# Performance work log

Measured on AMD Instinct MI355X. Metric: run time of the kernel, lower is better.

The kernel has to match this reference:

```python
import jax, jax.numpy as jnp
import numpy as np

E, H, V = 512, 1024, 32000
T_IN, T_DEC, B = 128, 128, 64
SOS = 1
WIPE_IDS = jnp.array([2, 3, 4])  # <EOS>, '\u56fe', '\u6298'


def gru_cell(x, h, Wih, Whh, bih, bhh):
    # torch nn.GRU cell math
    gi = x @ Wih.T + bih  # [B, 3H]
    gh = h @ Whh.T + bhh  # [B, 3H]
    i_r, i_z, i_n = jnp.split(gi, 3, axis=-1)
    h_r, h_z, h_n = jnp.split(gh, 3, axis=-1)
    r = jax.nn.sigmoid(i_r + h_r)
    z = jax.nn.sigmoid(i_z + h_z)
    n = jnp.tanh(i_n + r * h_n)
    return (1.0 - z) * n + z * h


def setup_inputs() -> dict:
    key = jax.random.key(0)
    ks = jax.random.split(key, 20)
    f = lambda k, shape: jax.random.normal(k, shape, jnp.float32) * 0.05
    inp = {
        'emb': f(ks[0], (V, E)),
        'enc_Wih': f(ks[1], (3 * H, E)), 'enc_Whh': f(ks[2], (3 * H, H)),
        'enc_bih': f(ks[3], (3 * H,)), 'enc_bhh': f(ks[4], (3 * H,)),
        'attn_W': f(ks[5], (T_IN, E + H)), 'attn_b': f(ks[6], (T_IN,)),
        'comb_W': f(ks[7], (H, E + H)), 'comb_b': f(ks[8], (H,)),
        'dec_Wih': f(ks[9], (3 * H, H)), 'dec_Whh': f(ks[10], (3 * H, H)),
        'dec_bih': f(ks[11], (3 * H,)), 'dec_bhh': f(ks[12], (3 * H,)),
        'out_W': f(ks[13], (V, H)), 'out_b': f(ks[14], (V,)),
        'src_tokens': jax.random.randint(ks[15], (B, T_IN), 0, V, jnp.int32),
        'tgt_tokens': jax.random.randint(ks[16], (B, T_DEC), 0, V, jnp.int32),
    }
    # pack_padded_sequence needs lengths sorted descending with max == T_IN
    sl = jax.random.randint(ks[17], (B,), 1, T_IN + 1, jnp.int32).at[0].set(T_IN)
    inp['src_lengths'] = jnp.sort(sl)[::-1]
    tl = jax.random.randint(ks[18], (B,), 1, T_DEC + 1, jnp.int32).at[0].set(T_DEC)
    inp['tgt_lengths'] = tl
    return inp


def reference(emb, enc_Wih, enc_Whh, enc_bih, enc_bhh, attn_W, attn_b,
              comb_W, comb_b, dec_Wih, dec_Whh, dec_bih, dec_bhh,
              out_W, out_b, src_tokens, src_lengths, tgt_tokens, tgt_lengths):
    # ---------------- Encoder (packed GRU semantics) ----------------
    x = emb[src_tokens]  # [B, T_IN, E]  (dropout is eval-mode identity)
    valid = jnp.arange(T_IN)[None, :] < src_lengths[:, None]  # [B, T_IN]

    def enc_step(h, inp):
        xt, vt = inp  # [B,E], [B]
        hn = gru_cell(xt, h, enc_Wih, enc_Whh, enc_bih, enc_bhh)
        h = jnp.where(vt[:, None], hn, h)          # freeze hidden past length
        out = jnp.where(vt[:, None], hn, 0.0)      # pad_packed zeros past length
        return h, out

    h0 = jnp.zeros((B, H), emb.dtype)
    enc_h, enc_out = jax.lax.scan(enc_step, h0, (x.transpose(1, 0, 2), valid.T))
    enc_out = enc_out.transpose(1, 0, 2)  # [B, T_IN, H]
    enc_out = jax.nn.log_softmax(enc_out, axis=1)  # LogSoftmax(dim=1) over time, as in source

    # ---------------- Attention decoder with teacher forcing ----------------
    sos = jnp.full((B,), SOS, src_tokens.dtype)

    def dec_step(carry, inp):
        h, prev = carry
        di, tgt_t = inp
        e = emb[prev]  # [B, E]
        union = jnp.concatenate([e, h], axis=-1)  # [B, E+H]
        aw = jax.nn.softmax(union @ attn_W.T + attn_b, axis=-1)  # [B, T_IN]
        info = jnp.einsum('bt,bth->bh', aw, enc_out)  # bmm
        comb = jax.nn.relu(jnp.concatenate([e, info], axis=-1) @ comb_W.T + comb_b)
        h = gru_cell(comb, h, dec_Wih, dec_Whh, dec_bih, dec_bhh)
        logits = h @ out_W.T + out_b  # [B, V]
        m = di < tgt_lengths  # [B] wipeEOS condition: now_len < length[i]
        wiped = jnp.where(m[:, None], 0.0, logits[:, WIPE_IDS])
        logits = logits.at[:, WIPE_IDS].set(wiped)
        pred_t = jnp.argmax(logits, axis=-1)
        ce = -jax.nn.log_softmax(logits, axis=-1)[jnp.arange(B), tgt_t]
        mf = m.astype(logits.dtype)
        step_loss = jnp.sum(ce * mf) / jnp.sum(mf)  # masked_select(...).mean()
        return (h, tgt_t), (pred_t, step_loss)

    (_, _), (preds, losses) = jax.lax.scan(
        dec_step, (enc_h, sos), (jnp.arange(T_DEC), tgt_tokens.T))
    return preds.T, jnp.sum(losses)
```

## Files before the change

kernel.cpp:

```cpp
#include <hip/hip_runtime.h>
#include <math.h>

typedef long long i64;

#define B_    64
#define TIN   128
#define TDEC  128
#define E_    512
#define H_    1024
#define V_    32000
#define H3    3072
#define EH    1536
#define NROWS 8192
#define BH    (B_ * H_)

__device__ inline unsigned int ordf(float v) {
  unsigned int u = __float_as_uint(v);
  return (u & 0x80000000u) ? ~u : (u | 0x80000000u);
}

__device__ __forceinline__ void fma16(float acc[4][4], float4 s, float4 w) {
  acc[0][0] = fmaf(s.x, w.x, acc[0][0]); acc[0][1] = fmaf(s.x, w.y, acc[0][1]);
  acc[0][2] = fmaf(s.x, w.z, acc[0][2]); acc[0][3] = fmaf(s.x, w.w, acc[0][3]);
  acc[1][0] = fmaf(s.y, w.x, acc[1][0]); acc[1][1] = fmaf(s.y, w.y, acc[1][1]);
  acc[1][2] = fmaf(s.y, w.z, acc[1][2]); acc[1][3] = fmaf(s.y, w.w, acc[1][3]);
  acc[2][0] = fmaf(s.z, w.x, acc[2][0]); acc[2][1] = fmaf(s.z, w.y, acc[2][1]);
  acc[2][2] = fmaf(s.z, w.z, acc[2][2]); acc[2][3] = fmaf(s.z, w.w, acc[2][3]);
  acc[3][0] = fmaf(s.w, w.x, acc[3][0]); acc[3][1] = fmaf(s.w, w.y, acc[3][1]);
  acc[3][2] = fmaf(s.w, w.z, acc[3][2]); acc[3][3] = fmaf(s.w, w.w, acc[3][3]);
}

__global__ void diag_fill(float* __restrict__ out, int n, float val) {
  int i = blockIdx.x * blockDim.x + threadIdx.x;
  if (i < n) out[i] = val;
}

__global__ void init_ws(float* __restrict__ hbuf, unsigned long long* __restrict__ amaxkey,
                        float* __restrict__ sumexp) {
  int i = blockIdx.x * blockDim.x + threadIdx.x;
  if (i < 2 * B_ * H_) hbuf[i] = 0.f;
  if (i < NROWS) { amaxkey[i] = 0ull; sumexp[i] = 0.f; }
}

__global__ void prep_tokens(const int* __restrict__ src, const int* __restrict__ tgt,
                            int* __restrict__ tok_src, int* __restrict__ tok_prev) {
  int r = blockIdx.x * blockDim.x + threadIdx.x;
  if (r >= NROWS) return;
  int t = r >> 6, b = r & 63;
  tok_src[r]  = src[b * TIN + t];
  tok_prev[r] = (t == 0) ? 1 : tgt[b * TDEC + (t - 1)];
}

__global__ __launch_bounds__(256)
void gemm_gather(const float* __restrict__ emb, const int* __restrict__ tok,
                 const float* __restrict__ W, int wstride,
                 const float* __restrict__ bias,
                 float* __restrict__ C, int ldc) {
  __shared__ float As[32][132];
  __shared__ float Bs[32][136];
  __shared__ int toks[128];
  const int tid = threadIdx.x;
  const int tx = tid & 15, ty = tid >> 4;
  const int r0 = blockIdx.y * 128, n0 = blockIdx.x * 128;
  if (tid < 128) toks[tid] = tok[r0 + tid];
  __syncthreads();
  float acc[8][8];
#pragma unroll
  for (int i = 0; i < 8; ++i)
#pragma unroll
    for (int j = 0; j < 8; ++j) acc[i][j] = 0.f;

  for (int k0 = 0; k0 < E_; k0 += 32) {
#pragma unroll
    for (int j = 0; j < 4; ++j) {
      int s = tid + 256 * j;
      int m = s >> 3, k4 = (s & 7) << 2;
      float4 v = *reinterpret_cast<const float4*>(&emb[(i64)toks[m] * E_ + k0 + k4]);
      As[k4 + 0][m] = v.x; As[k4 + 1][m] = v.y; As[k4 + 2][m] = v.z; As[k4 + 3][m] = v.w;
      float4 u = *reinterpret_cast<const float4*>(&W[(i64)(n0 + m) * wstride + k0 + k4]);
      Bs[k4 + 0][m] = u.x; Bs[k4 + 1][m] = u.y; Bs[k4 + 2][m] = u.z; Bs[k4 + 3][m] = u.w;
    }
    __syncthreads();
#pragma unroll
    for (int k = 0; k < 32; ++k) {
      float a[8], b[8];
      *(float4*)&a[0] = *(float4*)&As[k][ty * 4];
      *(float4*)&a[4] = *(float4*)&As[k][64 + ty * 4];
      *(float4*)&b[0] = *(float4*)&Bs[k][tx * 4];
      *(float4*)&b[4] = *(float4*)&Bs[k][64 + tx * 4];
#pragma unroll
      for (int i = 0; i < 8; ++i)
#pragma unroll
        for (int j = 0; j < 8; ++j)
          acc[i][j] = fmaf(a[i], b[j], acc[i][j]);
    }
    __syncthreads();
  }
#pragma unroll
  for (int i = 0; i < 8; ++i) {
    int rl = (i < 4) ? (ty * 4 + i) : (64 + ty * 4 + i - 4);
    int r = r0 + rl;
#pragma unroll
    for (int j = 0; j < 8; ++j) {
      int cl = (j < 4) ? (tx * 4 + j) : (64 + tx * 4 + j - 4);
      int c = n0 + cl;
      C[(i64)r * ldc + c] = acc[i][j] + bias[c];
    }
  }
}

__global__ __launch_bounds__(512)
void enc_step2(const float* __restrict__ h_prev, float* __restrict__ h_next,
               const float* __restrict__ emb, const int* __restrict__ tokS,
               const float* __restrict__ Wih, const float* __restrict__ Whh,
               const float* __restrict__ bih, const float* __restrict__ bhh,
               const int* __restrict__ src_len, float* __restrict__ EncRaw, int t) {
  __shared__ float S[64][68];
  __shared__ float WL[64 * 32];
  __shared__ float red[8 * 1024];
  __shared__ int toks[64];
  const int tid = threadIdx.x;
  const int n0 = blockIdx.x * 4;
  const int bg = tid & 15, ac = (tid >> 4) & 3, ks = tid >> 6;
  const int b0 = bg * 4;
  if (tid < 64) toks[tid] = tokS[t * B_ + tid];
  float acc[4][4] = {{0}};
  for (int ch = 0; ch < 24; ++ch) {
    const bool isE = ch < 8;
    const int k0 = (isE ? ch : ch - 8) * 64;
    __syncthreads();
    {
      int b = tid & 63, kb = (tid >> 6) * 8;
      const float* src = isE ? &emb[(i64)toks[b] * E_ + k0 + kb]
                             : &h_prev[(i64)b * H_ + k0 + kb];
      float4 v0 = *(const float4*)src;
      float4 v1 = *(const float4*)(src + 4);
      S[kb + 0][b] = v0.x; S[kb + 1][b] = v0.y; S[kb + 2][b] = v0.z; S[kb + 3][b] = v0.w;
      S[kb + 4][b] = v1.x; S[kb + 5][b] = v1.y; S[kb + 6][b] = v1.z; S[kb + 7][b] = v1.w;
    }
    if (tid < 192) {
      int lin = tid * 4;
      int row12 = lin >> 6, k4 = lin & 63;
      int m = row12 >> 2, c = row12 & 3;
      const float* W = isE ? Wih : Whh;
      const int K = isE ? E_ : H_;
      float4 w = *(const float4*)&W[(i64)(m * H_ + n0 + c) * K + k0 + k4];
      int slot = ((m ^ ((k4 >> 2) & 7)) << 2) + c;
      WL[(k4 + 0) * 32 + slot] = w.x;
      WL[(k4 + 1) * 32 + slot] = w.y;
      WL[(k4 + 2) * 32 + slot] = w.z;
      WL[(k4 + 3) * 32 + slot] = w.w;
    }
    __syncthreads();
    const bool active = (ac < 2) || (ac == 2 && isE) || (ac == 3 && !isE);
    if (active) {
      const int m = (ac < 2) ? ac : 2;
#pragma unroll
      for (int kk = ks * 8; kk < ks * 8 + 8; ++kk) {
        float4 sv = *(float4*)&S[kk][b0];
        float4 wv = *(float4*)&WL[kk * 32 + ((m ^ ((kk >> 2) & 7)) << 2)];
        fma16(acc, sv, wv);
      }
    }
  }
  __syncthreads();
#pragma unroll
  for (int bi = 0; bi < 4; ++bi)
#pragma unroll
    for (int c = 0; c < 4; ++c)
      red[ks * 1024 + ac * 256 + c * 64 + b0 + bi] = acc[bi][c];
  __syncthreads();
  if (tid < 256) {
    int b = tid & 63, c = tid >> 6, col = n0 + c;
    float sr = 0, sz = 0, gin = 0, ghn = 0;
#pragma unroll
    for (int k2 = 0; k2 < 8; ++k2) {
      sr  += red[k2 * 1024 +   0 + c * 64 + b];
      sz  += red[k2 * 1024 + 256 + c * 64 + b];
      gin += red[k2 * 1024 + 512 + c * 64 + b];
      ghn += red[k2 * 1024 + 768 + c * 64 + b];
    }
    float r = 1.f / (1.f + expf(-(sr + bih[col] + bhh[col])));
    float z = 1.f / (1.f + expf(-(sz + bih[H_ + col] + bhh[H_ + col])));
    float nn = tanhf(gin + bih[2 * H_ + col] + r * (ghn + bhh[2 * H_ + col]));
    float hpv = h_prev[(i64)b * H_ + col];
    float hnew = (1.f - z) * nn + z * hpv;
    bool valid = t < src_len[b];
    h_next[(i64)b * H_ + col] = valid ? hnew : hpv;
    EncRaw[((i64)b * TIN + t) * H_ + col] = valid ? hnew : 0.f;
  }
}

__global__ void ls_time(float* __restrict__ Enc) {
  int idx = blockIdx.x * blockDim.x + threadIdx.x;
  int b = idx >> 10, c = idx & 1023;
  const i64 base = (i64)b * TIN * H_ + c;
  float M = -INFINITY;
  for (int t = 0; t < TIN; ++t) M = fmaxf(M, Enc[base + (i64)t * H_]);
  float S = 0.f;
  for (int t = 0; t < TIN; ++t) S += expf(Enc[base + (i64)t * H_] - M);
  float lg = M + logf(S);
  for (int t = 0; t < TIN; ++t) Enc[base + (i64)t * H_] -= lg;
}

__global__ __launch_bounds__(512)
void attn_info2(const float* __restrict__ h_prev, const float* __restrict__ Ae,
                const float* __restrict__ attn_W, const float* __restrict__ EncLS,
                float* __restrict__ info, int t) {
  __shared__ float hl[H_];
  __shared__ float sc[TIN];
  __shared__ float inf2[512];
  const int b = blockIdx.x & 63, quarter = blockIdx.x >> 6;
  const int tid = threadIdx.x;
  if (tid < 256) {
    float4 v = *(const float4*)&h_prev[(i64)b * H_ + tid * 4];
    *(float4*)&hl[tid * 4] = v;
  }
  __syncthreads();
  const int w = tid >> 6, lane = tid & 63;
#pragma unroll
  for (int si = 0; si < 16; ++si) {
    int s = w * 16 + si;
    float p = 0.f;
#pragma unroll
    for (int jj = 0; jj < 16; ++jj) {
      int j = jj * 64 + lane;
      p = fmaf(hl[j], attn_W[(i64)s * EH + E_ + j], p);
    }
#pragma unroll
    for (int off = 32; off > 0; off >>= 1) p += __shfl_down(p, off);
    if (lane == 0) sc[s] = p + Ae[((i64)t * B_ + b) * TIN + s];
  }
  __syncthreads();
  if (tid < 64) {
    float v0 = sc[tid], v1 = sc[tid + 64];
    float mx = fmaxf(v0, v1);
#pragma unroll
    for (int off = 32; off > 0; off >>= 1) mx = fmaxf(mx, __shfl_xor(mx, off));
    float e0 = expf(v0 - mx), e1 = expf(v1 - mx);
    float ss = e0 + e1;
#pragma unroll
    for (int off = 32; off > 0; off >>= 1) ss += __shfl_xor(ss, off);
    sc[tid] = e0 / ss; sc[tid + 64] = e1 / ss;
  }
  __syncthreads();
  {
    int c = quarter * 256 + (tid & 255);
    int th = tid >> 8;
    float acc = 0.f;
    for (int t2 = th * 64; t2 < th * 64 + 64; ++t2)
      acc = fmaf(sc[t2], EncLS[((i64)b * TIN + t2) * H_ + c], acc);
    inf2[tid] = acc;
    __syncthreads();
    if (th == 0) info[(i64)b * H_ + c] = acc + inf2[tid + 256];
  }
}

__global__ __launch_bounds__(512)
void comb2(const float* __restrict__ info, const float* __restrict__ emb,
           const int* __restrict__ tokP, const float* __restrict__ comb_W,
           const float* __restrict__ comb_b, float* __restrict__ comb, int t) {
  __shared__ float S[64][68];
  __shared__ float WB[64 * 20];
  __shared__ float red[8 * 256];
  __shared__ int toks[64];
  const int tid = threadIdx.x;
  const int n0 = blockIdx.x * 4;
  const int bg = tid & 15, cs = (tid >> 4) & 3, ks = tid >> 6;
  const int b0 = bg * 4;
  if (tid < 64) toks[tid] = tokP[t * B_ + tid];
  float acc[4] = {0, 0, 0, 0};
  for (int ch = 0; ch < 24; ++ch) {
    const bool isE = ch < 8;
    const int k0 = (isE ? ch : ch - 8) * 64;
    __syncthreads();
    {
      int b = tid & 63, kb = (tid >> 6) * 8;
      const float* src = isE ? &emb[(i64)toks[b] * E_ + k0 + kb]
                             : &info[(i64)b * H_ + k0 + kb];
      float4 v0 = *(const float4*)src;
      float4 v1 = *(const float4*)(src + 4);
      S[kb + 0][b] = v0.x; S[kb + 1][b] = v0.y; S[kb + 2][b] = v0.z; S[kb + 3][b] = v0.w;
      S[kb + 4][b] = v1.x; S[kb + 5][b] = v1.y; S[kb + 6][b] = v1.z; S[kb + 7][b] = v1.w;
    }
    if (tid < 64) {
      int k = tid;
      i64 koff = (i64)(isE ? 0 : E_) + k0 + k;
      float4 w;
      w.x = comb_W[(i64)(n0 + 0) * EH + koff];
      w.y = comb_W[(i64)(n0 + 1) * EH + koff];
      w.z = comb_W[(i64)(n0 + 2) * EH + koff];
      w.w = comb_W[(i64)(n0 + 3) * EH + koff];
      *(float4*)&WB[k * 20] = w;
    }
    __syncthreads();
#pragma unroll
    for (int kk = ks * 8; kk < ks * 8 + 8; ++kk) {
      float4 sv = *(float4*)&S[kk][b0];
      float wv = WB[kk * 20 + cs];
      acc[0] = fmaf(sv.x, wv, acc[0]);
      acc[1] = fmaf(sv.y, wv, acc[1]);
      acc[2] = fmaf(sv.z, wv, acc[2]);
      acc[3] = fmaf(sv.w, wv, acc[3]);
    }
  }
  __syncthreads();
#pragma unroll
  for (int bi = 0; bi < 4; ++bi)
    red[ks * 256 + cs * 64 + b0 + bi] = acc[bi];
  __syncthreads();
  if (tid < 256) {
    int b = tid & 63, c = tid >> 6;
    float s = comb_b[n0 + c];
#pragma unroll
    for (int k2 = 0; k2 < 8; ++k2) s += red[k2 * 256 + c * 64 + b];
    comb[(i64)b * H_ + n0 + c] = fmaxf(s, 0.f);
  }
}

__global__ __launch_bounds__(512)
void dec_gru2(const float* __restrict__ h_prev, const float* __restrict__ comb,
              const float* __restrict__ Wih, const float* __restrict__ Whh,
              const float* __restrict__ bih, const float* __restrict__ bhh,
              float* __restrict__ h_out) {
  __shared__ float S1[64][68];
  __shared__ float S2[64][68];
  __shared__ float WL[64 * 32];
  __shared__ float red[8 * 1024];
  const int tid = threadIdx.x;
  const int n0 = blockIdx.x * 4;
  const int bg = tid & 15, ac = (tid >> 4) & 3, ks = tid >> 6;
  const int b0 = bg * 4;
  float acc[4][4] = {{0}};
  for (int ch = 0; ch < 16; ++ch) {
    const int k0 = ch * 64;
    __syncthreads();
    {
      int b = tid & 63, kb = (tid >> 6) * 8;
      const float* s1 = &h_prev[(i64)b * H_ + k0 + kb];
      const float* s2 = &comb[(i64)b * H_ + k0 + kb];
      float4 v0 = *(const float4*)s1, v1 = *(const float4*)(s1 + 4);
      S1[kb + 0][b] = v0.x; S1[kb + 1][b] = v0.y; S1[kb + 2][b] = v0.z; S1[kb + 3][b] = v0.w;
      S1[kb + 4][b] = v1.x; S1[kb + 5][b] = v1.y; S1[kb + 6][b] = v1.z; S1[kb + 7][b] = v1.w;
      float4 u0 = *(const float4*)s2, u1 = *(const float4*)(s2 + 4);
      S2[kb + 0][b] = u0.x; S2[kb + 1][b] = u0.y; S2[kb + 2][b] = u0.z; S2[kb + 3][b] = u0.w;
      S2[kb + 4][b] = u1.x; S2[kb + 5][b] = u1.y; S2[kb + 6][b] = u1.z; S2[kb + 7][b] = u1.w;
    }
    if (tid < 384) {
      int lin = tid * 4;
      int row24 = lin >> 6, k4 = lin & 63;
      int m = row24 >> 2, c = row24 & 3;
      int g = m >> 1;
      const float* W = (m & 1) ? Wih : Whh;
      float4 w = *(const float4*)&W[(i64)(g * H_ + n0 + c) * H_ + k0 + k4];
      int slot = ((m ^ ((k4 >> 2) & 7)) << 2) + c;
      WL[(k4 + 0) * 32 + slot] = w.x;
      WL[(k4 + 1) * 32 + slot] = w.y;
      WL[(k4 + 2) * 32 + slot] = w.z;
      WL[(k4 + 3) * 32 + slot] = w.w;
    }
    __syncthreads();
    if (ac < 2) {
#pragma unroll
      for (int kk = ks * 8; kk < ks * 8 + 8; ++kk) {
        int key = (kk >> 2) & 7;
        float4 h4 = *(float4*)&S1[kk][b0];
        float4 c4 = *(float4*)&S2[kk][b0];
        float4 wh = *(float4*)&WL[kk * 32 + (((2 * ac) ^ key) << 2)];
        float4 wi = *(float4*)&WL[kk * 32 + (((2 * ac + 1) ^ key) << 2)];
        fma16(acc, h4, wh);
        fma16(acc, c4, wi);
      }
    } else if (ac == 2) {
#pragma unroll
      for (int kk = ks * 8; kk < ks * 8 + 8; ++kk) {
        int key = (kk >> 2) & 7;
        float4 c4 = *(float4*)&S2[kk][b0];
        float4 wi = *(float4*)&WL[kk * 32 + ((5 ^ key) << 2)];
        fma16(acc, c4, wi);
      }
    } else {
#pragma unroll
      for (int kk = ks * 8; kk < ks * 8 + 8; ++kk) {
        int key = (kk >> 2) & 7;
        float4 h4 = *(float4*)&S1[kk][b0];
        float4 wh = *(float4*)&WL[kk * 32 + ((4 ^ key) << 2)];
        fma16(acc, h4, wh);
      }
    }
  }
  __syncthreads();
#pragma unroll
  for (int bi = 0; bi < 4; ++bi)
#pragma unroll
    for (int c = 0; c < 4; ++c)
      red[ks * 1024 + ac * 256 + c * 64 + b0 + bi] = acc[bi][c];
  __syncthreads();
  if (tid < 256) {
    int b = tid & 63, c = tid >> 6, col = n0 + c;
    float sr = 0, sz = 0, gin = 0, ghn = 0;
#pragma unroll
    for (int k2 = 0; k2 < 8; ++k2) {
      sr  += red[k2 * 1024 +   0 + c * 64 + b];
      sz  += red[k2 * 1024 + 256 + c * 64 + b];
      gin += red[k2 * 1024 + 512 + c * 64 + b];
      ghn += red[k2 * 1024 + 768 + c * 64 + b];
    }
    float r = 1.f / (1.f + expf(-(sr + bih[col] + bhh[col])));
    float z = 1.f / (1.f + expf(-(sz + bih[H_ + col] + bhh[H_ + col])));
    float nn = tanhf(gin + bih[2 * H_ + col] + r * (ghn + bhh[2 * H_ + col]));
    float hpv = h_prev[(i64)b * H_ + col];
    h_out[(i64)b * H_ + col] = (1.f - z) * nn + z * hpv;
  }
}

__global__ __launch_bounds__(256)
void logits_fused(const float* __restrict__ A, const float* __restrict__ Wout,
                  const float* __restrict__ outb, const int* __restrict__ tlen,
                  unsigned long long* __restrict__ amaxkey, float* __restrict__ sumexp) {
  __shared__ union {
    struct { float As[32][132]; float Bs[32][136]; } g;
    struct { float redm[128][17]; int redi[128][17]; float reds[128][17]; } r;
  } sh;
  const int tid = threadIdx.x;
  const int tx = tid & 15, ty = tid >> 4;
  const int r0 = blockIdx.y * 128, n0 = blockIdx.x * 128;
  float acc[8][8];
#pragma unroll
  for (int i = 0; i < 8; ++i)
#pragma unroll
    for (int j = 0; j < 8; ++j) acc[i][j] = 0.f;

  for (int k0 = 0; k0 < H_; k0 += 32) {
#pragma unroll
    for (int j = 0; j < 4; ++j) {
      int s = tid + 256 * j;
      int m = s >> 3, k4 = (s & 7) << 2;
      float4 v = *reinterpret_cast<const float4*>(&A[(i64)(r0 + m) * H_ + k0 + k4]);
      sh.g.As[k4 + 0][m] = v.x; sh.g.As[k4 + 1][m] = v.y;
      sh.g.As[k4 + 2][m] = v.z; sh.g.As[k4 + 3][m] = v.w;
      float4 u = *reinterpret_cast<const float4*>(&Wout[(i64)(n0 + m) * H_ + k0 + k4]);
      sh.g.Bs[k4 + 0][m] = u.x; sh.g.Bs[k4 + 1][m] = u.y;
      sh.g.Bs[k4 + 2][m] = u.z; sh.g.Bs[k4 + 3][m] = u.w;
    }
    __syncthreads();
#pragma unroll
    for (int k = 0; k < 32; ++k) {
      float a[8], b[8];
      *(float4*)&a[0] = *(float4*)&sh.g.As[k][ty * 4];
      *(float4*)&a[4] = *(float4*)&sh.g.As[k][64 + ty * 4];
      *(float4*)&b[0] = *(float4*)&sh.g.Bs[k][tx * 4];
      *(float4*)&b[4] = *(float4*)&sh.g.Bs[k][64 + tx * 4];
#pragma unroll
      for (int i = 0; i < 8; ++i)
#pragma unroll
        for (int j = 0; j < 8; ++j)
          acc[i][j] = fmaf(a[i], b[j], acc[i][j]);
    }
    __syncthreads();
  }

  int cols[8], rloc[8];
#pragma unroll
  for (int j = 0; j < 8; ++j) cols[j] = n0 + ((j < 4) ? (tx * 4 + j) : (64 + tx * 4 + j - 4));
#pragma unroll
  for (int i = 0; i < 8; ++i) rloc[i] = (i < 4) ? (ty * 4 + i) : (64 + ty * 4 + i - 4);

#pragma unroll
  for (int i = 0; i < 8; ++i) {
    int r = r0 + rloc[i];
    int t = r >> 6, b = r & 63;
    bool m = t < tlen[b];
    float lm = -INFINITY; int li = 0x7fffffff; float ls = 0.f;
#pragma unroll
    for (int j = 0; j < 8; ++j) {
      float v = acc[i][j] + outb[cols[j]];
      if (m && cols[j] >= 2 && cols[j] <= 4) v = 0.f;
      ls += expf(v);
      if (v > lm || (v == lm && cols[j] < li)) { lm = v; li = cols[j]; }
    }
    sh.r.redm[rloc[i]][tx] = lm; sh.r.redi[rloc[i]][tx] = li; sh.r.reds[rloc[i]][tx] = ls;
  }
  __syncthreads();
  if (tid < 128) {
    float M = -INFINITY; int I = 0x7fffffff; float S = 0.f;
#pragma unroll
    for (int x = 0; x < 16; ++x) {
      float v = sh.r.redm[tid][x]; int id = sh.r.redi[tid][x];
      if (v > M || (v == M && id < I)) { M = v; I = id; }
      S += sh.r.reds[tid][x];
    }
    unsigned long long key = ((unsigned long long)ordf(M) << 32) | (0xFFFFFFFFu - (unsigned)I);
    atomicMax(&amaxkey[r0 + tid], key);
    atomicAdd(&sumexp[r0 + tid], S);
  }
}

__global__ void tlogit_kernel(const float* __restrict__ Hd, const float* __restrict__ Wout,
                              const float* __restrict__ outb, const int* __restrict__ tgt,
                              const int* __restrict__ tlen, float* __restrict__ tlog) {
  const int tid = threadIdx.x;
  const int w = tid >> 6, lane = tid & 63;
  const int r = blockIdx.x * 4 + w;
  const int t = r >> 6, b = r & 63;
  const int tg = tgt[b * TDEC + t];
  float p = 0.f;
#pragma unroll
  for (int jj = 0; jj < 16; ++jj) {
    int j = jj * 64 + lane;
    p = fmaf(Hd[(i64)r * H_ + j], Wout[(i64)tg * H_ + j], p);
  }
#pragma unroll
  for (int off = 32; off > 0; off >>= 1) p += __shfl_down(p, off);
  if (lane == 0) {
    float v = p + outb[tg];
    if ((t < tlen[b]) && tg >= 2 && tg <= 4) v = 0.f;
    tlog[r] = v;
  }
}

__global__ void merge_kernel(const unsigned long long* __restrict__ amaxkey,
                             const float* __restrict__ sumexp,
                             const float* __restrict__ tlog,
                             const int* __restrict__ tlen,
                             float* __restrict__ out, float* __restrict__ loss_t) {
  const int t = blockIdx.x, b = threadIdx.x;
  const int r = t * 64 + b;
  unsigned long long key = amaxkey[r];
  int I = (int)(0xFFFFFFFFu - (unsigned)(key & 0xFFFFFFFFull));
  float lse = logf(sumexp[r]);
  float ce = lse - tlog[r];
  bool m = t < tlen[b];
  out[b * TDEC + t] = (float)I;
  float num = m ? ce : 0.f;
  float den = m ? 1.f : 0.f;
#pragma unroll
  for (int off = 32; off > 0; off >>= 1) {
    num += __shfl_down(num, off);
    den += __shfl_down(den, off);
  }
  if (b == 0) loss_t[t] = num / den;
}

__global__ void loss_sum(const float* __restrict__ loss_t, float* __restrict__ out) {
  const int tid = threadIdx.x;
  float v = loss_t[tid];
#pragma unroll
  for (int off = 32; off > 0; off >>= 1) v += __shfl_down(v, off);
  __shared__ float ps[2];
  if ((tid & 63) == 0) ps[tid >> 6] = v;
  __syncthreads();
  if (tid == 0) out[B_ * TDEC] = ps[0] + ps[1];
}

extern "C" void kernel_launch(void* const* d_in, const int* in_sizes, int n_in,
                              void* d_out, int out_size, void* d_ws, size_t ws_size,
                              hipStream_t stream) {
  const float* emb     = (const float*)d_in[0];
  const float* enc_Wih = (const float*)d_in[1];
  const float* enc_Whh = (const float*)d_in[2];
  const float* enc_bih = (const float*)d_in[3];
  const float* enc_bhh = (const float*)d_in[4];
  const float* attn_W  = (const float*)d_in[5];
  const float* attn_b  = (const float*)d_in[6];
  const float* comb_W  = (const float*)d_in[7];
  const float* comb_b  = (const float*)d_in[8];
  const float* dec_Wih = (const float*)d_in[9];
  const float* dec_Whh = (const float*)d_in[10];
  const float* dec_bih = (const float*)d_in[11];
  const float* dec_bhh = (const float*)d_in[12];
  const float* out_W   = (const float*)d_in[13];
  const float* out_b   = (const float*)d_in[14];
  const int* src_tok = (const int*)d_in[15];
  const int* tgt_tok;
  const int* src_len;
  const int* tgt_len;
  if (in_sizes[16] == B_ * TDEC) {
    tgt_tok = (const int*)d_in[16];
    src_len = (const int*)d_in[17];
    tgt_len = (const int*)d_in[18];
  } else {
    src_len = (const int*)d_in[16];
    tgt_len = (const int*)d_in[17];
    tgt_tok = (const int*)d_in[18];
  }
  float* out = (float*)d_out;
  char* wsb = (char*)d_ws;
  size_t off = 0;
  auto alloc = [&](size_t bytes) { void* p = wsb + off; off += (bytes + 255) & ~(size_t)255; return p; };

  float* EncLS = (float*)alloc((size_t)NROWS * H_ * 4);
  float* hbuf  = (float*)alloc(2ull * B_ * H_ * 4);
  float* Ae    = (float*)alloc((size_t)NROWS * TIN * 4);
  float* Hdec  = (float*)alloc((size_t)NROWS * H_ * 4);
  float* info  = (float*)alloc((size_t)B_ * H_ * 4);
  float* comb  = (float*)alloc((size_t)B_ * H_ * 4);
  unsigned long long* amaxkey = (unsigned long long*)alloc((size_t)NROWS * 8);
  float* sumexp = (float*)alloc((size_t)NROWS * 4);
  float* tlog  = (float*)alloc((size_t)NROWS * 4);
  float* lossT = (float*)alloc(TDEC * 4);
  int* tokS    = (int*)alloc(NROWS * 4);
  int* tokP    = (int*)alloc(NROWS * 4);

  if (off > ws_size) {
    diag_fill<<<(out_size + 255) / 256, 256, 0, stream>>>(out, out_size, (float)ws_size);
    return;
  }

  init_ws<<<512, 256, 0, stream>>>(hbuf, amaxkey, sumexp);
  prep_tokens<<<32, 256, 0, stream>>>(src_tok, tgt_tok, tokS, tokP);
  gemm_gather<<<dim3(1, 64), 256, 0, stream>>>(emb, tokP, attn_W, EH, attn_b, Ae, TIN);

  for (int t = 0; t < TIN; ++t) {
    const float* hp = hbuf + (size_t)(t & 1) * BH;
    float* hn = hbuf + (size_t)((t + 1) & 1) * BH;
    enc_step2<<<256, 512, 0, stream>>>(hp, hn, emb, tokS, enc_Wih, enc_Whh,
                                       enc_bih, enc_bhh, src_len, EncLS, t);
  }
  ls_time<<<256, 256, 0, stream>>>(EncLS);

  for (int t = 0; t < TDEC; ++t) {
    const float* hp = (t == 0) ? hbuf : (Hdec + (i64)(t - 1) * BH);
    attn_info2<<<256, 512, 0, stream>>>(hp, Ae, attn_W, EncLS, info, t);
    comb2<<<256, 512, 0, stream>>>(info, emb, tokP, comb_W, comb_b, comb, t);
    dec_gru2<<<256, 512, 0, stream>>>(hp, comb, dec_Wih, dec_Whh, dec_bih, dec_bhh,
                                      Hdec + (i64)t * BH);
  }

  logits_fused<<<dim3(250, 64), 256, 0, stream>>>(Hdec, out_W, out_b, tgt_len, amaxkey, sumexp);
  tlogit_kernel<<<2048, 256, 0, stream>>>(Hdec, out_W, out_b, tgt_tok, tgt_len, tlog);
  merge_kernel<<<128, 64, 0, stream>>>(amaxkey, sumexp, tlog, tgt_len, out, lossT);
  loss_sum<<<1, 128, 0, stream>>>(lossT, out);
}
```

Measured before the change: 36.11 ms.

## Replace per-timestep kernel launches with persistent kernels using grid barriers

The encoder loop (128 launches) and the decoder loop (384 launches) each become one persistent kernel of 256 blocks. The kernel steps through time internally and synchronises all blocks with an atomic-counter grid barrier. The aim is to remove per-launch overhead and the kernel-boundary drains between dependent stages. The barrier relies on all 256 blocks being co-resident, otherwise it can deadlock, and each barrier spins on a global atomic.

```diff
diff --git a/kernel.cpp b/kernel.cpp
--- a/kernel.cpp
+++ b/kernel.cpp
@@ -30,16 +30,30 @@
   acc[3][2] = fmaf(s.w, w.z, acc[3][2]); acc[3][3] = fmaf(s.w, w.w, acc[3][3]);
 }
 
+__device__ __forceinline__ void grid_bar(int* bar, int target_mult) {
+  __syncthreads();
+  if (threadIdx.x == 0) {
+    __threadfence();
+    __hip_atomic_fetch_add(bar, 1, __ATOMIC_RELEASE, __HIP_MEMORY_SCOPE_AGENT);
+    const int target = target_mult * (int)gridDim.x;
+    while (__hip_atomic_load(bar, __ATOMIC_ACQUIRE, __HIP_MEMORY_SCOPE_AGENT) < target)
+      __builtin_amdgcn_s_sleep(1);
+    __threadfence();
+  }
+  __syncthreads();
+}
+
 __global__ void diag_fill(float* __restrict__ out, int n, float val) {
   int i = blockIdx.x * blockDim.x + threadIdx.x;
   if (i < n) out[i] = val;
 }
 
 __global__ void init_ws(float* __restrict__ hbuf, unsigned long long* __restrict__ amaxkey,
-                        float* __restrict__ sumexp) {
+                        float* __restrict__ sumexp, int* __restrict__ bars) {
   int i = blockIdx.x * blockDim.x + threadIdx.x;
   if (i < 2 * B_ * H_) hbuf[i] = 0.f;
   if (i < NROWS) { amaxkey[i] = 0ull; sumexp[i] = 0.f; }
+  if (i < 2) bars[i] = 0;
 }
 
 __global__ void prep_tokens(const int* __restrict__ src, const int* __restrict__ tgt,
@@ -110,84 +124,97 @@
 }
 
 __global__ __launch_bounds__(512)
-void enc_step2(const float* __restrict__ h_prev, float* __restrict__ h_next,
-               const float* __restrict__ emb, const int* __restrict__ tokS,
-               const float* __restrict__ Wih, const float* __restrict__ Whh,
-               const float* __restrict__ bih, const float* __restrict__ bhh,
-               const int* __restrict__ src_len, float* __restrict__ EncRaw, int t) {
-  __shared__ float S[64][68];
-  __shared__ float WL[64 * 32];
-  __shared__ float red[8 * 1024];
-  __shared__ int toks[64];
+void enc_persist(float* __restrict__ hbufs, const float* __restrict__ emb,
+                 const int* __restrict__ tokS,
+                 const float* __restrict__ Wih, const float* __restrict__ Whh,
+                 const float* __restrict__ bih, const float* __restrict__ bhh,
+                 const int* __restrict__ src_len, float* __restrict__ EncRaw,
+                 int* __restrict__ bar) {
+  __shared__ union {
+    struct {
+      float S[64][68];
+      float WL[64 * 32];
+      float red[8 * 1024];
+      int toks[64];
+    } e;
+  } sh;
   const int tid = threadIdx.x;
   const int n0 = blockIdx.x * 4;
   const int bg = tid & 15, ac = (tid >> 4) & 3, ks = tid >> 6;
   const int b0 = bg * 4;
-  if (tid < 64) toks[tid] = tokS[t * B_ + tid];
-  float acc[4][4] = {{0}};
-  for (int ch = 0; ch < 24; ++ch) {
-    const bool isE = ch < 8;
-    const int k0 = (isE ? ch : ch - 8) * 64;
+
+  for (int t = 0; t < TIN; ++t) {
+    const float* h_prev = hbufs + (size_t)(t & 1) * BH;
+    float* h_next = hbufs + (size_t)((t + 1) & 1) * BH;
+    if (tid < 64) sh.e.toks[tid] = tokS[t * B_ + tid];
+    float acc[4][4] = {{0}};
+    for (int ch = 0; ch < 24; ++ch) {
+      const bool isE = ch < 8;
+      const int k0 = (isE ? ch : ch - 8) * 64;
+      __syncthreads();
+      {
+        int b = tid & 63, kb = (tid >> 6) * 8;
+        const float* src = isE ? &emb[(i64)sh.e.toks[b] * E_ + k0 + kb]
+                               : &h_prev[(i64)b * H_ + k0 + kb];
+        float4 v0 = *(const float4*)src;
+        float4 v1 = *(const float4*)(src + 4);
+        sh.e.S[kb + 0][b] = v0.x; sh.e.S[kb + 1][b] = v0.y;
+        sh.e.S[kb + 2][b] = v0.z; sh.e.S[kb + 3][b] = v0.w;
+        sh.e.S[kb + 4][b] = v1.x; sh.e.S[kb + 5][b] = v1.y;
+        sh.e.S[kb + 6][b] = v1.z; sh.e.S[kb + 7][b] = v1.w;
+      }
+      if (tid < 192) {
+        int lin = tid * 4;
+        int row12 = lin >> 6, k4 = lin & 63;
+        int m = row12 >> 2, c = row12 & 3;
+        const float* W = isE ? Wih : Whh;
+        const int K = isE ? E_ : H_;
+        float4 w = *(const float4*)&W[(i64)(m * H_ + n0 + c) * K + k0 + k4];
+        int slot = ((m ^ ((k4 >> 2) & 7)) << 2) + c;
+        sh.e.WL[(k4 + 0) * 32 + slot] = w.x;
+        sh.e.WL[(k4 + 1) * 32 + slot] = w.y;
+        sh.e.WL[(k4 + 2) * 32 + slot] = w.z;
+        sh.e.WL[(k4 + 3) * 32 + slot] = w.w;
+      }
+      __syncthreads();
+      const bool active = (ac < 2) || (ac == 2 && isE) || (ac == 3 && !isE);
+      if (active) {
+        const int m = (ac < 2) ? ac : 2;
+#pragma unroll
+        for (int kk = ks * 8; kk < ks * 8 + 8; ++kk) {
+          float4 sv = *(float4*)&sh.e.S[kk][b0];
+          float4 wv = *(float4*)&sh.e.WL[kk * 32 + ((m ^ ((kk >> 2) & 7)) << 2)];
+          fma16(acc, sv, wv);
+        }
+      }
+    }
     __syncthreads();
-    {
-      int b = tid & 63, kb = (tid >> 6) * 8;
-      const float* src = isE ? &emb[(i64)toks[b] * E_ + k0 + kb]
-                             : &h_prev[(i64)b * H_ + k0 + kb];
-      float4 v0 = *(const float4*)src;
-      float4 v1 = *(const float4*)(src + 4);
-      S[kb + 0][b] = v0.x; S[kb + 1][b] = v0.y; S[kb + 2][b] = v0.z; S[kb + 3][b] = v0.w;
-      S[kb + 4][b] = v1.x; S[kb + 5][b] = v1.y; S[kb + 6][b] = v1.z; S[kb + 7][b] = v1.w;
-    }
-    if (tid < 192) {
-      int lin = tid * 4;
-      int row12 = lin >> 6, k4 = lin & 63;
-      int m = row12 >> 2, c = row12 & 3;
-      const float* W = isE ? Wih : Whh;
-      const int K = isE ? E_ : H_;
-      float4 w = *(const float4*)&W[(i64)(m * H_ + n0 + c) * K + k0 + k4];
-      int slot = ((m ^ ((k4 >> 2) & 7)) << 2) + c;
-      WL[(k4 + 0) * 32 + slot] = w.x;
-      WL[(k4 + 1) * 32 + slot] = w.y;
-      WL[(k4 + 2) * 32 + slot] = w.z;
-      WL[(k4 + 3) * 32 + slot] = w.w;
-    }
+#pragma unroll
+    for (int bi = 0; bi < 4; ++bi)
+#pragma unroll
+      for (int c = 0; c < 4; ++c)
+        sh.e.red[ks * 1024 + ac * 256 + c * 64 + b0 + bi] = acc[bi][c];
     __syncthreads();
-    const bool active = (ac < 2) || (ac == 2 && isE) || (ac == 3 && !isE);
-    if (active) {
-      const int m = (ac < 2) ? ac : 2;
-#pragma unroll
-      for (int kk = ks * 8; kk < ks * 8 + 8; ++kk) {
-        float4 sv = *(float4*)&S[kk][b0];
-        float4 wv = *(float4*)&WL[kk * 32 + ((m ^ ((kk >> 2) & 7)) << 2)];
-        fma16(acc, sv, wv);
-      }
-    }
-  }
-  __syncthreads();
-#pragma unroll
-  for (int bi = 0; bi < 4; ++bi)
-#pragma unroll
-    for (int c = 0; c < 4; ++c)
-      red[ks * 1024 + ac * 256 + c * 64 + b0 + bi] = acc[bi][c];
-  __syncthreads();
-  if (tid < 256) {
-    int b = tid & 63, c = tid >> 6, col = n0 + c;
-    float sr = 0, sz = 0, gin = 0, ghn = 0;
-#pragma unroll
-    for (int k2 = 0; k2 < 8; ++k2) {
-      sr  += red[k2 * 1024 +   0 + c * 64 + b];
-      sz  += red[k2 * 1024 + 256 + c * 64 + b];
-      gin += red[k2 * 1024 + 512 + c * 64 + b];
-      ghn += red[k2 * 1024 + 768 + c * 64 + b];
-    }
-    float r = 1.f / (1.f + expf(-(sr + bih[col] + bhh[col])));
-    float z = 1.f / (1.f + expf(-(sz + bih[H_ + col] + bhh[H_ + col])));
-    float nn = tanhf(gin + bih[2 * H_ + col] + r * (ghn + bhh[2 * H_ + col]));
-    float hpv = h_prev[(i64)b * H_ + col];
-    float hnew = (1.f - z) * nn + z * hpv;
-    bool valid = t < src_len[b];
-    h_next[(i64)b * H_ + col] = valid ? hnew : hpv;
-    EncRaw[((i64)b * TIN + t) * H_ + col] = valid ? hnew : 0.f;
+    if (tid < 256) {
+      int b = tid & 63, c = tid >> 6, col = n0 + c;
+      float sr = 0, sz = 0, gin = 0, ghn = 0;
+#pragma unroll
+      for (int k2 = 0; k2 < 8; ++k2) {
+        sr  += sh.e.red[k2 * 1024 +   0 + c * 64 + b];
+        sz  += sh.e.red[k2 * 1024 + 256 + c * 64 + b];
+        gin += sh.e.red[k2 * 1024 + 512 + c * 64 + b];
+        ghn += sh.e.red[k2 * 1024 + 768 + c * 64 + b];
+      }
+      float r = 1.f / (1.f + expf(-(sr + bih[col] + bhh[col])));
+      float z = 1.f / (1.f + expf(-(sz + bih[H_ + col] + bhh[H_ + col])));
+      float nn = tanhf(gin + bih[2 * H_ + col] + r * (ghn + bhh[2 * H_ + col]));
+      float hpv = h_prev[(i64)b * H_ + col];
+      float hnew = (1.f - z) * nn + z * hpv;
+      bool valid = t < src_len[b];
+      h_next[(i64)b * H_ + col] = valid ? hnew : hpv;
+      EncRaw[((i64)b * TIN + t) * H_ + col] = valid ? hnew : 0.f;
+    }
+    grid_bar(bar, t + 1);
   }
 }
 
@@ -204,213 +231,221 @@
 }
 
 __global__ __launch_bounds__(512)
-void attn_info2(const float* __restrict__ h_prev, const float* __restrict__ Ae,
-                const float* __restrict__ attn_W, const float* __restrict__ EncLS,
-                float* __restrict__ info, int t) {
-  __shared__ float hl[H_];
-  __shared__ float sc[TIN];
-  __shared__ float inf2[512];
-  const int b = blockIdx.x & 63, quarter = blockIdx.x >> 6;
+void dec_persist(const float* __restrict__ h0, float* __restrict__ Hdec,
+                 const float* __restrict__ emb, const int* __restrict__ tokP,
+                 const float* __restrict__ Ae, const float* __restrict__ attn_W,
+                 const float* __restrict__ EncLS,
+                 const float* __restrict__ comb_W, const float* __restrict__ comb_b,
+                 const float* __restrict__ Wih, const float* __restrict__ Whh,
+                 const float* __restrict__ bih, const float* __restrict__ bhh,
+                 float* __restrict__ info, float* __restrict__ comb,
+                 int* __restrict__ bar) {
+  __shared__ union {
+    struct { float hl[H_]; float sc[TIN]; float inf2[512]; } a;
+    struct { float S[64][68]; float WB[64 * 20]; float red[8 * 256]; int toks[64]; } b;
+    struct { float S1[64][68]; float S2[64][68]; float WL[64 * 32]; float red[8 * 1024]; } c;
+  } sh;
   const int tid = threadIdx.x;
-  if (tid < 256) {
-    float4 v = *(const float4*)&h_prev[(i64)b * H_ + tid * 4];
-    *(float4*)&hl[tid * 4] = v;
-  }
-  __syncthreads();
-  const int w = tid >> 6, lane = tid & 63;
-#pragma unroll
-  for (int si = 0; si < 16; ++si) {
-    int s = w * 16 + si;
-    float p = 0.f;
-#pragma unroll
-    for (int jj = 0; jj < 16; ++jj) {
-      int j = jj * 64 + lane;
-      p = fmaf(hl[j], attn_W[(i64)s * EH + E_ + j], p);
-    }
-#pragma unroll
-    for (int off = 32; off > 0; off >>= 1) p += __shfl_down(p, off);
-    if (lane == 0) sc[s] = p + Ae[((i64)t * B_ + b) * TIN + s];
-  }
-  __syncthreads();
-  if (tid < 64) {
-    float v0 = sc[tid], v1 = sc[tid + 64];
-    float mx = fmaxf(v0, v1);
-#pragma unroll
-    for (int off = 32; off > 0; off >>= 1) mx = fmaxf(mx, __shfl_xor(mx, off));
-    float e0 = expf(v0 - mx), e1 = expf(v1 - mx);
-    float ss = e0 + e1;
-#pragma unroll
-    for (int off = 32; off > 0; off >>= 1) ss += __shfl_xor(ss, off);
-    sc[tid] = e0 / ss; sc[tid + 64] = e1 / ss;
-  }
-  __syncthreads();
-  {
-    int c = quarter * 256 + (tid & 255);
-    int th = tid >> 8;
-    float acc = 0.f;
-    for (int t2 = th * 64; t2 < th * 64 + 64; ++t2)
-      acc = fmaf(sc[t2], EncLS[((i64)b * TIN + t2) * H_ + c], acc);
-    inf2[tid] = acc;
-    __syncthreads();
-    if (th == 0) info[(i64)b * H_ + c] = acc + inf2[tid + 256];
-  }
-}
-
-__global__ __launch_bounds__(512)
-void comb2(const float* __restrict__ info, const float* __restrict__ emb,
-           const int* __restrict__ tokP, const float* __restrict__ comb_W,
-           const float* __restrict__ comb_b, float* __restrict__ comb, int t) {
-  __shared__ float S[64][68];
-  __shared__ float WB[64 * 20];
-  __shared__ float red[8 * 256];
-  __shared__ int toks[64];
-  const int tid = threadIdx.x;
-  const int n0 = blockIdx.x * 4;
-  const int bg = tid & 15, cs = (tid >> 4) & 3, ks = tid >> 6;
-  const int b0 = bg * 4;
-  if (tid < 64) toks[tid] = tokP[t * B_ + tid];
-  float acc[4] = {0, 0, 0, 0};
-  for (int ch = 0; ch < 24; ++ch) {
-    const bool isE = ch < 8;
-    const int k0 = (isE ? ch : ch - 8) * 64;
-    __syncthreads();
+  int sync_i = 0;
+
+  for (int t = 0; t < TDEC; ++t) {
+    const float* h_prev = (t == 0) ? h0 : (Hdec + (i64)(t - 1) * BH);
+
     {
-      int b = tid & 63, kb = (tid >> 6) * 8;
-      const float* src = isE ? &emb[(i64)toks[b] * E_ + k0 + kb]
-                             : &info[(i64)b * H_ + k0 + kb];
-      float4 v0 = *(const float4*)src;
-      float4 v1 = *(const float4*)(src + 4);
-      S[kb + 0][b] = v0.x; S[kb + 1][b] = v0.y; S[kb + 2][b] = v0.z; S[kb + 3][b] = v0.w;
-      S[kb + 4][b] = v1.x; S[kb + 5][b] = v1.y; S[kb + 6][b] = v1.z; S[kb + 7][b] = v1.w;
-    }
-    if (tid < 64) {
-      int k = tid;
-      i64 koff = (i64)(isE ? 0 : E_) + k0 + k;
-      float4 w;
-      w.x = comb_W[(i64)(n0 + 0) * EH + koff];
-      w.y = comb_W[(i64)(n0 + 1) * EH + koff];
-      w.z = comb_W[(i64)(n0 + 2) * EH + koff];
-      w.w = comb_W[(i64)(n0 + 3) * EH + koff];
-      *(float4*)&WB[k * 20] = w;
-    }
-    __syncthreads();
-#pragma unroll
-    for (int kk = ks * 8; kk < ks * 8 + 8; ++kk) {
-      float4 sv = *(float4*)&S[kk][b0];
-      float wv = WB[kk * 20 + cs];
-      acc[0] = fmaf(sv.x, wv, acc[0]);
-      acc[1] = fmaf(sv.y, wv, acc[1]);
-      acc[2] = fmaf(sv.z, wv, acc[2]);
-      acc[3] = fmaf(sv.w, wv, acc[3]);
-    }
-  }
-  __syncthreads();
-#pragma unroll
-  for (int bi = 0; bi < 4; ++bi)
-    red[ks * 256 + cs * 64 + b0 + bi] = acc[bi];
-  __syncthreads();
-  if (tid < 256) {
-    int b = tid & 63, c = tid >> 6;
-    float s = comb_b[n0 + c];
-#pragma unroll
-    for (int k2 = 0; k2 < 8; ++k2) s += red[k2 * 256 + c * 64 + b];
-    comb[(i64)b * H_ + n0 + c] = fmaxf(s, 0.f);
-  }
-}
-
-__global__ __launch_bounds__(512)
-void dec_gru2(const float* __restrict__ h_prev, const float* __restrict__ comb,
-              const float* __restrict__ Wih, const float* __restrict__ Whh,
-              const float* __restrict__ bih, const float* __restrict__ bhh,
-              float* __restrict__ h_out) {
-  __shared__ float S1[64][68];
-  __shared__ float S2[64][68];
-  __shared__ float WL[64 * 32];
-  __shared__ float red[8 * 1024];
-  const int tid = threadIdx.x;
-  const int n0 = blockIdx.x * 4;
-  const int bg = tid & 15, ac = (tid >> 4) & 3, ks = tid >> 6;
-  const int b0 = bg * 4;
-  float acc[4][4] = {{0}};
-  for (int ch = 0; ch < 16; ++ch) {
-    const int k0 = ch * 64;
-    __syncthreads();
+      const int b = blockIdx.x & 63, quarter = blockIdx.x >> 6;
+      if (tid < 256) {
+        float4 v = *(const float4*)&h_prev[(i64)b * H_ + tid * 4];
+        *(float4*)&sh.a.hl[tid * 4] = v;
+      }
+      __syncthreads();
+      const int w = tid >> 6, lane = tid & 63;
+#pragma unroll
+      for (int si = 0; si < 16; ++si) {
+        int s = w * 16 + si;
+        float p = 0.f;
+#pragma unroll
+        for (int jj = 0; jj < 16; ++jj) {
+          int j = jj * 64 + lane;
+          p = fmaf(sh.a.hl[j], attn_W[(i64)s * EH + E_ + j], p);
+        }
+#pragma unroll
+        for (int off = 32; off > 0; off >>= 1) p += __shfl_down(p, off);
+        if (lane == 0) sh.a.sc[s] = p + Ae[((i64)t * B_ + b) * TIN + s];
+      }
+      __syncthreads();
+      if (tid < 64) {
+        float v0 = sh.a.sc[tid], v1 = sh.a.sc[tid + 64];
+        float mx = fmaxf(v0, v1);
+#pragma unroll
+        for (int off = 32; off > 0; off >>= 1) mx = fmaxf(mx, __shfl_xor(mx, off));
+        float e0 = expf(v0 - mx), e1 = expf(v1 - mx);
+        float ss = e0 + e1;
+#pragma unroll
+        for (int off = 32; off > 0; off >>= 1) ss += __shfl_xor(ss, off);
+        sh.a.sc[tid] = e0 / ss; sh.a.sc[tid + 64] = e1 / ss;
+      }
+      __syncthreads();
+      {
+        int c = quarter * 256 + (tid & 255);
+        int th = tid >> 8;
+        float acc = 0.f;
+        for (int t2 = th * 64; t2 < th * 64 + 64; ++t2)
+          acc = fmaf(sh.a.sc[t2], EncLS[((i64)b * TIN + t2) * H_ + c], acc);
+        sh.a.inf2[tid] = acc;
+        __syncthreads();
+        if (th == 0) info[(i64)b * H_ + c] = acc + sh.a.inf2[tid + 256];
+      }
+    }
+    grid_bar(bar, ++sync_i);
+
     {
-      int b = tid & 63, kb = (tid >> 6) * 8;
-      const float* s1 = &h_prev[(i64)b * H_ + k0 + kb];
-      const float* s2 = &comb[(i64)b * H_ + k0 + kb];
-      float4 v0 = *(const float4*)s1, v1 = *(const float4*)(s1 + 4);
-      S1[kb + 0][b] = v0.x; S1[kb + 1][b] = v0.y; S1[kb + 2][b] = v0.z; S1[kb + 3][b] = v0.w;
-      S1[kb + 4][b] = v1.x; S1[kb + 5][b] = v1.y; S1[kb + 6][b] = v1.z; S1[kb + 7][b] = v1.w;
-      float4 u0 = *(const float4*)s2, u1 = *(const float4*)(s2 + 4);
-      S2[kb + 0][b] = u0.x; S2[kb + 1][b] = u0.y; S2[kb + 2][b] = u0.z; S2[kb + 3][b] = u0.w;
-      S2[kb + 4][b] = u1.x; S2[kb + 5][b] = u1.y; S2[kb + 6][b] = u1.z; S2[kb + 7][b] = u1.w;
-    }
-    if (tid < 384) {
-      int lin = tid * 4;
-      int row24 = lin >> 6, k4 = lin & 63;
-      int m = row24 >> 2, c = row24 & 3;
-      int g = m >> 1;
-      const float* W = (m & 1) ? Wih : Whh;
-      float4 w = *(const float4*)&W[(i64)(g * H_ + n0 + c) * H_ + k0 + k4];
-      int slot = ((m ^ ((k4 >> 2) & 7)) << 2) + c;
-      WL[(k4 + 0) * 32 + slot] = w.x;
-      WL[(k4 + 1) * 32 + slot] = w.y;
-      WL[(k4 + 2) * 32 + slot] = w.z;
-      WL[(k4 + 3) * 32 + slot] = w.w;
-    }
-    __syncthreads();
-    if (ac < 2) {
-#pragma unroll
-      for (int kk = ks * 8; kk < ks * 8 + 8; ++kk) {
-        int key = (kk >> 2) & 7;
-        float4 h4 = *(float4*)&S1[kk][b0];
-        float4 c4 = *(float4*)&S2[kk][b0];
-        float4 wh = *(float4*)&WL[kk * 32 + (((2 * ac) ^ key) << 2)];
-        float4 wi = *(float4*)&WL[kk * 32 + (((2 * ac + 1) ^ key) << 2)];
-        fma16(acc, h4, wh);
-        fma16(acc, c4, wi);
-      }
-    } else if (ac == 2) {
-#pragma unroll
-      for (int kk = ks * 8; kk < ks * 8 + 8; ++kk) {
-        int key = (kk >> 2) & 7;
-        float4 c4 = *(float4*)&S2[kk][b0];
-        float4 wi = *(float4*)&WL[kk * 32 + ((5 ^ key) << 2)];
-        fma16(acc, c4, wi);
-      }
-    } else {
-#pragma unroll
-      for (int kk = ks * 8; kk < ks * 8 + 8; ++kk) {
-        int key = (kk >> 2) & 7;
-        float4 h4 = *(float4*)&S1[kk][b0];
-        float4 wh = *(float4*)&WL[kk * 32 + ((4 ^ key) << 2)];
-        fma16(acc, h4, wh);
-      }
-    }
-  }
-  __syncthreads();
-#pragma unroll
-  for (int bi = 0; bi < 4; ++bi)
-#pragma unroll
-    for (int c = 0; c < 4; ++c)
-      red[ks * 1024 + ac * 256 + c * 64 + b0 + bi] = acc[bi][c];
-  __syncthreads();
-  if (tid < 256) {
-    int b = tid & 63, c = tid >> 6, col = n0 + c;
-    float sr = 0, sz = 0, gin = 0, ghn = 0;
-#pragma unroll
-    for (int k2 = 0; k2 < 8; ++k2) {
-      sr  += red[k2 * 1024 +   0 + c * 64 + b];
-      sz  += red[k2 * 1024 + 256 + c * 64 + b];
-      gin += red[k2 * 1024 + 512 + c * 64 + b];
-      ghn += red[k2 * 1024 + 768 + c * 64 + b];
-    }
-    float r = 1.f / (1.f + expf(-(sr + bih[col] + bhh[col])));
-    float z = 1.f / (1.f + expf(-(sz + bih[H_ + col] + bhh[H_ + col])));
-    float nn = tanhf(gin + bih[2 * H_ + col] + r * (ghn + bhh[2 * H_ + col]));
-    float hpv = h_prev[(i64)b * H_ + col];
-    h_out[(i64)b * H_ + col] = (1.f - z) * nn + z * hpv;
+      const int n0 = blockIdx.x * 4;
+      const int bg = tid & 15, cs = (tid >> 4) & 3, ks = tid >> 6;
+      const int b0 = bg * 4;
+      if (tid < 64) sh.b.toks[tid] = tokP[t * B_ + tid];
+      float acc[4] = {0, 0, 0, 0};
+      for (int ch = 0; ch < 24; ++ch) {
+        const bool isE = ch < 8;
+        const int k0 = (isE ? ch : ch - 8) * 64;
+        __syncthreads();
+        {
+          int b = tid & 63, kb = (tid >> 6) * 8;
+          const float* src = isE ? &emb[(i64)sh.b.toks[b] * E_ + k0 + kb]
+                                 : &info[(i64)b * H_ + k0 + kb];
+          float4 v0 = *(const float4*)src;
+          float4 v1 = *(const float4*)(src + 4);
+          sh.b.S[kb + 0][b] = v0.x; sh.b.S[kb + 1][b] = v0.y;
+          sh.b.S[kb + 2][b] = v0.z; sh.b.S[kb + 3][b] = v0.w;
+          sh.b.S[kb + 4][b] = v1.x; sh.b.S[kb + 5][b] = v1.y;
+          sh.b.S[kb + 6][b] = v1.z; sh.b.S[kb + 7][b] = v1.w;
+        }
+        if (tid < 64) {
+          int k = tid;
+          i64 koff = (i64)(isE ? 0 : E_) + k0 + k;
+          float4 w;
+          w.x = comb_W[(i64)(n0 + 0) * EH + koff];
+          w.y = comb_W[(i64)(n0 + 1) * EH + koff];
+          w.z = comb_W[(i64)(n0 + 2) * EH + koff];
+          w.w = comb_W[(i64)(n0 + 3) * EH + koff];
+          *(float4*)&sh.b.WB[k * 20] = w;
+        }
+        __syncthreads();
+#pragma unroll
+        for (int kk = ks * 8; kk < ks * 8 + 8; ++kk) {
+          float4 sv = *(float4*)&sh.b.S[kk][b0];
+          float wv = sh.b.WB[kk * 20 + cs];
+          acc[0] = fmaf(sv.x, wv, acc[0]);
+          acc[1] = fmaf(sv.y, wv, acc[1]);
+          acc[2] = fmaf(sv.z, wv, acc[2]);
+          acc[3] = fmaf(sv.w, wv, acc[3]);
+        }
+      }
+      __syncthreads();
+#pragma unroll
+      for (int bi = 0; bi < 4; ++bi)
+        sh.b.red[ks * 256 + cs * 64 + b0 + bi] = acc[bi];
+      __syncthreads();
+      if (tid < 256) {
+        int b = tid & 63, c = tid >> 6;
+        float s = comb_b[n0 + c];
+#pragma unroll
+        for (int k2 = 0; k2 < 8; ++k2) s += sh.b.red[k2 * 256 + c * 64 + b];
+        comb[(i64)b * H_ + n0 + c] = fmaxf(s, 0.f);
+      }
+    }
+    grid_bar(bar, ++sync_i);
+
+    {
+      const int n0 = blockIdx.x * 4;
+      const int bg = tid & 15, ac = (tid >> 4) & 3, ks = tid >> 6;
+      const int b0 = bg * 4;
+      float acc[4][4] = {{0}};
+      for (int ch = 0; ch < 16; ++ch) {
+        const int k0 = ch * 64;
+        __syncthreads();
+        {
+          int b = tid & 63, kb = (tid >> 6) * 8;
+          const float* s1 = &h_prev[(i64)b * H_ + k0 + kb];
+          const float* s2 = &comb[(i64)b * H_ + k0 + kb];
+          float4 v0 = *(const float4*)s1, v1 = *(const float4*)(s1 + 4);
+          sh.c.S1[kb + 0][b] = v0.x; sh.c.S1[kb + 1][b] = v0.y;
+          sh.c.S1[kb + 2][b] = v0.z; sh.c.S1[kb + 3][b] = v0.w;
+          sh.c.S1[kb + 4][b] = v1.x; sh.c.S1[kb + 5][b] = v1.y;
+          sh.c.S1[kb + 6][b] = v1.z; sh.c.S1[kb + 7][b] = v1.w;
+          float4 u0 = *(const float4*)s2, u1 = *(const float4*)(s2 + 4);
+          sh.c.S2[kb + 0][b] = u0.x; sh.c.S2[kb + 1][b] = u0.y;
+          sh.c.S2[kb + 2][b] = u0.z; sh.c.S2[kb + 3][b] = u0.w;
+          sh.c.S2[kb + 4][b] = u1.x; sh.c.S2[kb + 5][b] = u1.y;
+          sh.c.S2[kb + 6][b] = u1.z; sh.c.S2[kb + 7][b] = u1.w;
+        }
+        if (tid < 384) {
+          int lin = tid * 4;
+          int row24 = lin >> 6, k4 = lin & 63;
+          int m = row24 >> 2, c = row24 & 3;
+          int g = m >> 1;
+          const float* W = (m & 1) ? Wih : Whh;
+          float4 w = *(const float4*)&W[(i64)(g * H_ + n0 + c) * H_ + k0 + k4];
+          int slot = ((m ^ ((k4 >> 2) & 7)) << 2) + c;
+          sh.c.WL[(k4 + 0) * 32 + slot] = w.x;
+          sh.c.WL[(k4 + 1) * 32 + slot] = w.y;
+          sh.c.WL[(k4 + 2) * 32 + slot] = w.z;
+          sh.c.WL[(k4 + 3) * 32 + slot] = w.w;
+        }
+        __syncthreads();
+        if (ac < 2) {
+#pragma unroll
+          for (int kk = ks * 8; kk < ks * 8 + 8; ++kk) {
+            int key = (kk >> 2) & 7;
+            float4 h4 = *(float4*)&sh.c.S1[kk][b0];
+            float4 c4 = *(float4*)&sh.c.S2[kk][b0];
+            float4 wh = *(float4*)&sh.c.WL[kk * 32 + (((2 * ac) ^ key) << 2)];
+            float4 wi = *(float4*)&sh.c.WL[kk * 32 + (((2 * ac + 1) ^ key) << 2)];
+            fma16(acc, h4, wh);
+            fma16(acc, c4, wi);
+          }
+        } else if (ac == 2) {
+#pragma unroll
+          for (int kk = ks * 8; kk < ks * 8 + 8; ++kk) {
+            int key = (kk >> 2) & 7;
+            float4 c4 = *(float4*)&sh.c.S2[kk][b0];
+            float4 wi = *(float4*)&sh.c.WL[kk * 32 + ((5 ^ key) << 2)];
+            fma16(acc, c4, wi);
+          }
+        } else {
+#pragma unroll
+          for (int kk = ks * 8; kk < ks * 8 + 8; ++kk) {
+            int key = (kk >> 2) & 7;
+            float4 h4 = *(float4*)&sh.c.S1[kk][b0];
+            float4 wh = *(float4*)&sh.c.WL[kk * 32 + ((4 ^ key) << 2)];
+            fma16(acc, h4, wh);
+          }
+        }
+      }
+      __syncthreads();
+#pragma unroll
+      for (int bi = 0; bi < 4; ++bi)
+#pragma unroll
+        for (int c = 0; c < 4; ++c)
+          sh.c.red[ks * 1024 + ac * 256 + c * 64 + b0 + bi] = acc[bi][c];
+      __syncthreads();
+      if (tid < 256) {
+        int b = tid & 63, c = tid >> 6, col = n0 + c;
+        float sr = 0, sz = 0, gin = 0, ghn = 0;
+#pragma unroll
+        for (int k2 = 0; k2 < 8; ++k2) {
+          sr  += sh.c.red[k2 * 1024 +   0 + c * 64 + b];
+          sz  += sh.c.red[k2 * 1024 + 256 + c * 64 + b];
+          gin += sh.c.red[k2 * 1024 + 512 + c * 64 + b];
+          ghn += sh.c.red[k2 * 1024 + 768 + c * 64 + b];
+        }
+        float r = 1.f / (1.f + expf(-(sr + bih[col] + bhh[col])));
+        float z = 1.f / (1.f + expf(-(sz + bih[H_ + col] + bhh[H_ + col])));
+        float nn = tanhf(gin + bih[2 * H_ + col] + r * (ghn + bhh[2 * H_ + col]));
+        float hpv = h_prev[(i64)b * H_ + col];
+        Hdec[(i64)t * BH + (i64)b * H_ + col] = (1.f - z) * nn + z * hpv;
+      }
+    }
+    grid_bar(bar, ++sync_i);
   }
 }
 
@@ -601,31 +636,24 @@
   float* lossT = (float*)alloc(TDEC * 4);
   int* tokS    = (int*)alloc(NROWS * 4);
   int* tokP    = (int*)alloc(NROWS * 4);
+  int* bars    = (int*)alloc(256);
 
   if (off > ws_size) {
     diag_fill<<<(out_size + 255) / 256, 256, 0, stream>>>(out, out_size, (float)ws_size);
     return;
   }
 
-  init_ws<<<512, 256, 0, stream>>>(hbuf, amaxkey, sumexp);
+  init_ws<<<512, 256, 0, stream>>>(hbuf, amaxkey, sumexp, bars);
   prep_tokens<<<32, 256, 0, stream>>>(src_tok, tgt_tok, tokS, tokP);
   gemm_gather<<<dim3(1, 64), 256, 0, stream>>>(emb, tokP, attn_W, EH, attn_b, Ae, TIN);
 
-  for (int t = 0; t < TIN; ++t) {
-    const float* hp = hbuf + (size_t)(t & 1) * BH;
-    float* hn = hbuf + (size_t)((t + 1) & 1) * BH;
-    enc_step2<<<256, 512, 0, stream>>>(hp, hn, emb, tokS, enc_Wih, enc_Whh,
-                                       enc_bih, enc_bhh, src_len, EncLS, t);
-  }
+  enc_persist<<<256, 512, 0, stream>>>(hbuf, emb, tokS, enc_Wih, enc_Whh,
+                                       enc_bih, enc_bhh, src_len, EncLS, &bars[0]);
   ls_time<<<256, 256, 0, stream>>>(EncLS);
 
-  for (int t = 0; t < TDEC; ++t) {
-    const float* hp = (t == 0) ? hbuf : (Hdec + (i64)(t - 1) * BH);
-    attn_info2<<<256, 512, 0, stream>>>(hp, Ae, attn_W, EncLS, info, t);
-    comb2<<<256, 512, 0, stream>>>(info, emb, tokP, comb_W, comb_b, comb, t);
-    dec_gru2<<<256, 512, 0, stream>>>(hp, comb, dec_Wih, dec_Whh, dec_bih, dec_bhh,
-                                      Hdec + (i64)t * BH);
-  }
+  dec_persist<<<256, 512, 0, stream>>>(hbuf, Hdec, emb, tokP, Ae, attn_W, EncLS,
+                                       comb_W, comb_b, dec_Wih, dec_Whh,
+                                       dec_bih, dec_bhh, info, comb, &bars[1]);
 
   logits_fused<<<dim3(250, 64), 256, 0, stream>>>(Hdec, out_W, out_b, tgt_len, amaxkey, sumexp);
   tlogit_kernel<<<2048, 256, 0, stream>>>(Hdec, out_W, out_b, tgt_tok, tgt_len, tlog);
```

After: 62.30 ms. 72.5% more time.
